# Kernel tuning notes

Measured on AMD Instinct MI355X. Metric: run time of the kernel, lower is better.

Reference implementation:

```python
import jax, jax.numpy as jnp
import numpy as np

K = 24            # neighbors
RBF_KERNELS = 16
RBF_GAMMA = 10.0
CUTOFF = 5.0
BN_EPS = 1e-5


def setup_inputs() -> dict:
    key = jax.random.key(0)
    ks = jax.random.split(key, 6)
    B, C, N = 16, 32, 2048
    x = jax.random.normal(ks[0], (B, C, N), dtype=jnp.float32)
    idx_base = (jnp.arange(B, dtype=jnp.int64) * N).reshape(B, 1, 1)
    att_w1 = jax.random.normal(ks[1], (64, 2 * C + RBF_KERNELS), dtype=jnp.float32) * 0.1
    att_w2 = jax.random.normal(ks[2], (1, 64), dtype=jnp.float32) * 0.1
    upd_w = jax.random.normal(ks[3], (64, C), dtype=jnp.float32) * 0.1
    bn_gamma = jnp.ones((64,), dtype=jnp.float32)
    bn_beta = jnp.zeros((64,), dtype=jnp.float32)
    res_w = jax.random.normal(ks[4], (64, C), dtype=jnp.float32) * 0.1
    return {"x": x, "idx_base": idx_base, "att_w1": att_w1, "att_w2": att_w2,
            "upd_w": upd_w, "bn_gamma": bn_gamma, "bn_beta": bn_beta, "res_w": res_w}


def _forward(x, att_w1, att_w2, upd_w, bn_gamma, bn_beta, res_w):
    B, C, N = x.shape
    centers = jnp.linspace(0.0, CUTOFF, RBF_KERNELS).astype(x.dtype)
    # pair[b,i,j] = -||x_i - x_j||^2  (negative squared distance)
    xx = jnp.sum(x * x, axis=1)                          # [B,N]
    dots = jnp.einsum('bcn,bcm->bnm', x, x)              # [B,N,N]
    pair = 2.0 * dots - xx[:, :, None] - xx[:, None, :]
    neg_d2, idx = jax.lax.top_k(pair, K)                 # [B,N,K] nearest neighbors
    dist = jnp.sqrt(jnp.maximum(-neg_d2, 1e-12))         # [B,N,K]
    xt = jnp.transpose(x, (0, 2, 1))                     # [B,N,C]
    neigh = xt[jnp.arange(B)[:, None, None], idx]        # [B,N,K,C] gather
    cent = jnp.broadcast_to(xt[:, :, None, :], (B, N, K, C))
    # RBF expansion of neighbor distances
    diff = dist[..., None] - centers                     # [B,N,K,RBF]
    rbf = jnp.clip(jnp.exp(-RBF_GAMMA * diff * diff), 1e-10, 1.0)
    # attention MLP (1x1 convs == per-edge dense layers)
    att_in = jnp.concatenate([cent, neigh, rbf], axis=-1)          # [B,N,K,2C+RBF]
    h = jax.nn.leaky_relu(jnp.einsum('bnkf,of->bnko', att_in, att_w1), 0.2)
    logits = jnp.einsum('bnko,o->bnk', h, att_w2[0])               # [B,N,K]
    att = jax.nn.softmax(logits, axis=-1)                          # softmax over K neighbors
    weighted = att[..., None] * neigh                              # [B,N,K,C]
    # update_ff: conv1x1 -> BatchNorm2d (batch stats over B,N,K) -> LeakyReLU(0.02)
    upd = jnp.einsum('bnkc,oc->bnko', weighted, upd_w)             # [B,N,K,64]
    mean = jnp.mean(upd, axis=(0, 1, 2))
    var = jnp.mean((upd - mean) ** 2, axis=(0, 1, 2))
    upd = (upd - mean) * jax.lax.rsqrt(var + BN_EPS) * bn_gamma + bn_beta
    upd = jax.nn.leaky_relu(upd, 0.02)
    res = jnp.einsum('bnkc,oc->bnko', neigh, res_w)                # residual projection
    feat = jnp.mean(upd + 0.1 * res, axis=2)                       # mean over K -> [B,N,64]
    return jnp.transpose(feat, (0, 2, 1))                          # [B,64,N]


def reference(x, idx_base, att_w1, att_w2, upd_w, bn_gamma, bn_beta, res_w):
    # idx_base is only needed for torch's flattened-gather trick; the per-batch
    # advanced-index gather above computes identical math.
    return _forward(x, att_w1, att_w2, upd_w, bn_gamma, bn_beta, res_w)
```

## Files before the change

### kernel.cpp

```cpp
#include <hip/hip_runtime.h>
#include <math.h>

#define B_   16
#define C_   32
#define N_   2048
#define K_   24
#define BNK_ (B_*N_*K_)

typedef float vf2 __attribute__((ext_vector_type(2)));
typedef __attribute__((ext_vector_type(8))) short bf16x8;
typedef __attribute__((ext_vector_type(4))) float f32x4;

#define WS_XT   0u
#define WS_XXD  1048576u
#define WS_XXF  1114112u
#define WS_IDX  1146880u
#define WS_D2   1933312u
#define WS_ATT  2719744u
#define WS_LOG  3506176u
#define WS_ST   4292608u
#define WS_AB   4292736u
#define WS_W    4292864u
#define WS_W2   4325632u
#define WS_Y    4358400u
#define WS_L    4358400u
#define WS_HL   10649856u

__device__ __forceinline__ unsigned short bf16rne(float f) {
  unsigned int u = __float_as_uint(f);
  return (unsigned short)((u + 0x7FFFu + ((u >> 16) & 1u)) >> 16);
}

__global__ __launch_bounds__(256) void k0_prep(const float* __restrict__ x,
                                               float* __restrict__ ws) {
  const int i = blockIdx.x;
  const int xcd = i & 7, j = i >> 3;
  const int b = 2 * xcd + (j & 1);
  const int half = j >> 1;
  const int t = (b << 11) + (half << 8) + threadIdx.x;
  const int n = t & 2047;
  const float* xp = x + ((size_t)b * C_ * N_) + n;
  float4* xt4 = (float4*)(ws + WS_XT + (size_t)t * C_);
  uint4*  hl  = (uint4*)(ws + WS_HL) + (size_t)t * 8;
  unsigned int hu[16], lu[16];
  double s = 0.0;
#pragma unroll
  for (int cg = 0; cg < 8; ++cg) {
    float4 v;
    v.x = xp[(size_t)(4*cg  ) * N_];
    v.y = xp[(size_t)(4*cg+1) * N_];
    v.z = xp[(size_t)(4*cg+2) * N_];
    v.w = xp[(size_t)(4*cg+3) * N_];
    xt4[cg] = v;
    s = fma((double)v.x, (double)v.x, s);
    s = fma((double)v.y, (double)v.y, s);
    s = fma((double)v.z, (double)v.z, s);
    s = fma((double)v.w, (double)v.w, s);
    unsigned short h0 = bf16rne(v.x), h1 = bf16rne(v.y);
    unsigned short h2 = bf16rne(v.z), h3 = bf16rne(v.w);
    float l0 = v.x - __uint_as_float((unsigned int)h0 << 16);
    float l1 = v.y - __uint_as_float((unsigned int)h1 << 16);
    float l2 = v.z - __uint_as_float((unsigned int)h2 << 16);
    float l3 = v.w - __uint_as_float((unsigned int)h3 << 16);
    hu[2*cg]   = (unsigned int)h0 | ((unsigned int)h1 << 16);
    hu[2*cg+1] = (unsigned int)h2 | ((unsigned int)h3 << 16);
    lu[2*cg]   = (unsigned int)bf16rne(l0) | ((unsigned int)bf16rne(l1) << 16);
    lu[2*cg+1] = (unsigned int)bf16rne(l2) | ((unsigned int)bf16rne(l3) << 16);
  }
#pragma unroll
  for (int q = 0; q < 4; ++q) {
    uint4 hv; hv.x = hu[4*q]; hv.y = hu[4*q+1]; hv.z = hu[4*q+2]; hv.w = hu[4*q+3];
    hl[q] = hv;
    uint4 lv; lv.x = lu[4*q]; lv.y = lu[4*q+1]; lv.z = lu[4*q+2]; lv.w = lu[4*q+3];
    hl[4+q] = lv;
  }
  ((double*)(ws + WS_XXD))[t] = s;
  ws[WS_XXF + t] = -0.5f * (float)s;
  ws[WS_W + t] = 0.f;
  ws[WS_W2 + t] = 0.f;
  if (t < 128) ws[WS_ST + t] = 0.f;
}

__global__ __launch_bounds__(256, 8) void k1a_mfma(float* __restrict__ ws) {
  __shared__ unsigned short tl[2][1024];
  const int lane = threadIdx.x & 63;
  const int wv   = __builtin_amdgcn_readfirstlane(threadIdx.x >> 6);
  const int i = blockIdx.x;
  const int xcd = i & 7, j = i >> 3;
  const int b = 2 * xcd + (j & 1);
  const int j2 = j >> 1;
  const int nblk = j2 >> 2;
  const int mq   = j2 & 3;
  const int l16 = lane & 15, lg = lane >> 4;

  const unsigned short* HL = (const unsigned short*)(ws + WS_HL) + ((size_t)b << 17);
  const int nrow = (nblk << 6) + (wv << 4) + l16;
  const bf16x8 bh = *(const bf16x8*)(HL + ((size_t)nrow << 6) + (lg << 3));
  const bf16x8 bl = *(const bf16x8*)(HL + ((size_t)nrow << 6) + 32 + (lg << 3));

  const int mbase = mq << 9;
  const float4* nxx = (const float4*)(ws + WS_XXF + (b << 11) + mbase);

  const int srow = lane >> 3;
  const int sslot = (lane & 7) ^ srow;
  const unsigned short* Sp = HL + ((size_t)(mbase + srow) << 6) + (sslot << 3);

  const int ah_off = (l16 << 6) + (((lg    ) ^ (l16 & 7)) << 3);
  const int al_off = (l16 << 6) + (((4 | lg) ^ (l16 & 7)) << 3);

  if (wv == 0) {
    __builtin_amdgcn_global_load_lds(
        (const __attribute__((address_space(1))) unsigned int*)(const void*)Sp,
        (__attribute__((address_space(3))) unsigned int*)(void*)&tl[0][0], 16, 0, 0);
    __builtin_amdgcn_global_load_lds(
        (const __attribute__((address_space(1))) unsigned int*)(const void*)(Sp + 512),
        (__attribute__((address_space(3))) unsigned int*)(void*)&tl[0][512], 16, 0, 0);
  }
  __syncthreads();

  float val[12];
#pragma unroll
  for (int j0 = 0; j0 < 12; ++j0) val[j0] = -3.4e38f;
  int id = mbase + (lg << 2);

#pragma unroll 2
  for (int t = 0; t < 32; ++t) {
    const int cur = t & 1;
    if (t < 31 && wv == (t & 3)) {
      const unsigned short* sp = Sp + ((size_t)(t + 1) << 10);
      __builtin_amdgcn_global_load_lds(
          (const __attribute__((address_space(1))) unsigned int*)(const void*)sp,
          (__attribute__((address_space(3))) unsigned int*)(void*)&tl[cur ^ 1][0], 16, 0, 0);
      __builtin_amdgcn_global_load_lds(
          (const __attribute__((address_space(1))) unsigned int*)(const void*)(sp + 512),
          (__attribute__((address_space(3))) unsigned int*)(void*)&tl[cur ^ 1][512], 16, 0, 0);
    }
    bf16x8 ah = *(const bf16x8*)(&tl[cur][ah_off]);
    bf16x8 al = *(const bf16x8*)(&tl[cur][al_off]);
    float4 xq = nxx[(t << 2) + lg];
    f32x4 acc;
    acc[0] = xq.x; acc[1] = xq.y; acc[2] = xq.z; acc[3] = xq.w;
    acc = __builtin_amdgcn_mfma_f32_16x16x32_bf16(ah, bh, acc, 0, 0, 0);
    acc = __builtin_amdgcn_mfma_f32_16x16x32_bf16(al, bh, acc, 0, 0, 0);
    acc = __builtin_amdgcn_mfma_f32_16x16x32_bf16(ah, bl, acc, 0, 0, 0);
#pragma unroll
    for (int r = 0; r < 4; ++r) {
      int sb = (__float_as_int(acc[r]) & ~2047) | (id + r);
      float sp2 = __int_as_float(sb);
#pragma unroll
      for (int j0 = 11; j0 >= 1; --j0)
        val[j0] = __builtin_amdgcn_fmed3f(val[j0 - 1], val[j0], sp2);
      val[0] = fmaxf(val[0], sp2);
    }
    id += 16;
    __syncthreads();
  }
  const int pg = (b << 5) + nblk;
  float* Lp = ws + WS_L +
      (((size_t)pg * 16 + (mq << 2) + lg) * 12) * 64 + (wv << 4) + l16;
#pragma unroll
  for (int j0 = 0; j0 < 12; ++j0) Lp[(size_t)j0 * 64] = val[j0];
}

__global__ __launch_bounds__(64) void k1b_sel(float* __restrict__ ws) {
  const float* xt = ws + WS_XT;
  const double* xxd = (const double*)(ws + WS_XXD);
  const int lane = threadIdx.x & 63;
  const int i = blockIdx.x;
  const int xcd = i & 7, j = i >> 3;
  const int b = 2 * xcd + (j & 1);
  const int sub = j >> 1;
  const int pg = (b << 5) + sub;
  const int bn = (b << 11) + (sub << 6) + lane;

  float val[28];
#pragma unroll
  for (int j0 = 0; j0 < 28; ++j0) val[j0] = -3.4e38f;
  const float* Lp = ws + WS_L + ((size_t)pg * 16 * 12) * 64 + lane;
#pragma unroll 4
  for (int t = 0; t < 192; ++t) {
    float sp = Lp[(size_t)t * 64];
#pragma unroll
    for (int j0 = 27; j0 >= 1; --j0)
      val[j0] = __builtin_amdgcn_fmed3f(val[j0 - 1], val[j0], sp);
    val[0] = fmaxf(val[0], sp);
  }

  double xnd[C_];
  {
    const float* p = xt + (size_t)bn * C_;
#pragma unroll
    for (int c = 0; c < C_; ++c) xnd[c] = (double)p[c];
  }
  double dl[K_];
#pragma unroll
  for (int j0 = 0; j0 < K_; ++j0) dl[j0] = -1.7e308;

#pragma unroll 1
  for (int j0 = 0; j0 < 28; ++j0) {
    const int m = __float_as_int(val[j0]) & 2047;
    const float* r = xt + ((size_t)((b << 11) + m)) * C_;
    double a0 = 0.0, a1 = 0.0;
#pragma unroll
    for (int c = 0; c < 16; ++c) {
      a0 = fma((double)r[c],      xnd[c],      a0);
      a1 = fma((double)r[c + 16], xnd[c + 16], a1);
    }
    double s = 2.0 * (a0 + a1) - xxd[(b << 11) + m];
    long long bits = (__double_as_longlong(s) & 0xFFFFFFFFFFFFF800ll) | (long long)m;
    double sp = __longlong_as_double(bits);
    if (sp > dl[K_ - 1]) {
      bool c2 = true;
#pragma unroll
      for (int jj = K_ - 1; jj >= 1; --jj) {
        bool c1 = sp > dl[jj - 1];
        dl[jj] = c1 ? dl[jj - 1] : (c2 ? sp : dl[jj]);
        c2 = c1;
      }
      if (c2) dl[0] = sp;
    }
  }

  int*   op = (int*)ws + WS_IDX + (size_t)bn * K_;
  float* dp = ws + WS_D2 + (size_t)bn * K_;
  const double xxn = xxd[bn];
#pragma unroll
  for (int rr = 0; rr < K_; ++rr) {
    long long bl = __double_as_longlong(dl[rr]);
    op[rr] = (int)(bl & 0x7FFll);
    dp[rr] = (float)(xxn - __longlong_as_double(bl & 0xFFFFFFFFFFFFF800ll));
  }
}

__global__ __launch_bounds__(256) void kY(const float* __restrict__ w1,
                                          const float* __restrict__ updw,
                                          const float* __restrict__ resw,
                                          float* __restrict__ ws) {
  const int lane = threadIdx.x & 63;
  const int wv   = __builtin_amdgcn_readfirstlane(threadIdx.x >> 6);
  const int i = blockIdx.x;
  const int xcd = i & 7, j = i >> 3;
  const int b = 2 * xcd + (j & 1);
  const int j2 = j >> 1;
  const int slot = (j2 << 2) | wv;
  const int s  = slot & 7;
  const int pg = slot >> 3;
  const int p = (b << 11) + (pg << 6) + lane;
  const float* xt = ws + WS_XT;

  float row[C_];
  {
    const float4* rp = (const float4*)(xt + (size_t)p * C_);
#pragma unroll
    for (int q = 0; q < 8; ++q) {
      float4 v = rp[q];
      row[4*q] = v.x; row[4*q+1] = v.y; row[4*q+2] = v.z; row[4*q+3] = v.w;
    }
  }
  const int part = s >> 1;
  const int hch  = (s & 1) * 32;
  const float* W   = (part == 0) ? w1 : (part == 1) ? (w1 + 32)
                   : (part == 2) ? updw : resw;
  const int stride = (part < 2) ? 80 : 32;
  float* yp = ws + WS_Y + (size_t)p * 256 + s * 32;
#pragma unroll 2
  for (int og = 0; og < 8; ++og) {
    float a[4] = {0.f, 0.f, 0.f, 0.f};
#pragma unroll
    for (int u = 0; u < 4; ++u) {
      const float* wr = W + (hch + 4 * og + u) * stride;
#pragma unroll
      for (int c = 0; c < C_; ++c) a[u] = fmaf(row[c], wr[c], a[u]);
    }
    float4 st; st.x = a[0]; st.y = a[1]; st.z = a[2]; st.w = a[3];
    ((float4*)yp)[og] = st;
  }
}

__global__ __launch_bounds__(256, 6) void k2_logits(const float* __restrict__ w1,
                                                    const float* __restrict__ w2,
                                                    float* __restrict__ ws) {
  const int lane = threadIdx.x & 63;
  const int wv   = __builtin_amdgcn_readfirstlane(threadIdx.x >> 6);
  const int i = blockIdx.x;
  const int xcd = i & 7, j = i >> 3;
  const int b = 2 * xcd + (j & 1);
  const int j2 = j >> 1;
  const int sub = j2 & 31;
  const int third = j2 >> 5;
  const int k0 = (third * 4 + wv) * 2;
  const int bn = (b << 11) + (sub << 6) + lane;
  const float* Y = ws + WS_Y;

  float rbf[2][16];
  int mk[2];
#pragma unroll
  for (int kk = 0; kk < 2; ++kk) {
    const int k = k0 + kk;
    mk[kk] = ((const int*)ws)[WS_IDX + (size_t)bn * K_ + k];
    const float dd = ws[WS_D2 + (size_t)bn * K_ + k];
    float dist = sqrtf(fmaxf(dd, 1e-12f));
#pragma unroll
    for (int r = 0; r < 16; ++r) {
      float t = dist - (float)r * (5.0f / 15.0f);
      float e = __expf(-10.f * t * t);
      rbf[kk][r] = fminf(fmaxf(e, 1e-10f), 1.0f);
    }
  }

  float lg[2] = {0.f, 0.f};
  const float4* bp = (const float4*)(Y + (size_t)bn * 256);
  const float4* yp0 = (const float4*)(Y + (size_t)((b << 11) + mk[0]) * 256 + 64);
  const float4* yp1 = (const float4*)(Y + (size_t)((b << 11) + mk[1]) * 256 + 64);
#pragma unroll
  for (int og = 0; og < 4; ++og) {
#pragma unroll
    for (int q = 0; q < 4; ++q) {
      float4 bv  = bp[og * 4 + q];
      float4 rv0 = yp0[og * 4 + q];
      float4 rv1 = yp1[og * 4 + q];
#pragma unroll
      for (int e = 0; e < 4; ++e) {
        const int o = og * 16 + q * 4 + e;
        const float be = (e == 0) ? bv.x : (e == 1) ? bv.y : (e == 2) ? bv.z : bv.w;
        const float r0 = (e == 0) ? rv0.x : (e == 1) ? rv0.y : (e == 2) ? rv0.z : rv0.w;
        const float r1 = (e == 0) ? rv1.x : (e == 1) ? rv1.y : (e == 2) ? rv1.z : rv1.w;
        float a0 = be + r0, a1 = be + r1;
#pragma unroll
        for (int r = 0; r < 16; ++r) {
          const float wv1 = w1[o * 80 + 64 + r];
          a0 = fmaf(rbf[0][r], wv1, a0);
          a1 = fmaf(rbf[1][r], wv1, a1);
        }
        float h0 = a0 > 0.f ? a0 : 0.2f * a0;
        float h1 = a1 > 0.f ? a1 : 0.2f * a1;
        lg[0] = fmaf(h0, w2[o], lg[0]);
        lg[1] = fmaf(h1, w2[o], lg[1]);
      }
    }
  }
#pragma unroll
  for (int kk = 0; kk < 2; ++kk)
    ws[WS_LOG + (size_t)(k0 + kk) * 32768 + bn] = lg[kk];
}

__global__ __launch_bounds__(256) void k2_softmax(float* __restrict__ ws) {
  __shared__ float h[4096];
  const int i = blockIdx.x;
  const int xcd = i & 7, j = i >> 3;
  const int b = 2 * xcd + (j & 1);
  const int half = j >> 1;
  const int bn = (b << 11) + (half << 8) + threadIdx.x;

#pragma unroll
  for (int q = 0; q < 16; ++q) h[threadIdx.x + (q << 8)] = 0.f;
  __syncthreads();

  float l[K_];
#pragma unroll
  for (int k = 0; k < K_; ++k) l[k] = ws[WS_LOG + (size_t)k * 32768 + bn];
  float mx = l[0];
#pragma unroll
  for (int k = 1; k < K_; ++k) mx = fmaxf(mx, l[k]);
  float den = 0.f;
#pragma unroll
  for (int k = 0; k < K_; ++k) { l[k] = __expf(l[k] - mx); den += l[k]; }
  const float inv = 1.f / den;
#pragma unroll
  for (int k = 0; k < K_; ++k) l[k] *= inv;

  float4* ap = (float4*)(ws + WS_ATT + (size_t)bn * K_);
#pragma unroll
  for (int q = 0; q < 6; ++q) {
    float4 v; v.x = l[4*q]; v.y = l[4*q+1]; v.z = l[4*q+2]; v.w = l[4*q+3];
    ap[q] = v;
  }
  const int* ip = (const int*)ws + WS_IDX + (size_t)bn * K_;
#pragma unroll
  for (int k = 0; k < K_; ++k) {
    const int mk = ip[k];
    atomicAdd(&h[mk], l[k]);
    atomicAdd(&h[2048 + mk], l[k] * l[k]);
  }
  __syncthreads();
#pragma unroll
  for (int q = 0; q < 8; ++q) {
    const int m = threadIdx.x + (q << 8);
    atomicAdd(ws + WS_W  + (b << 11) + m, h[m]);
    atomicAdd(ws + WS_W2 + (b << 11) + m, h[2048 + m]);
  }
}

__global__ __launch_bounds__(256) void k2b_stats(float* __restrict__ ws) {
  __shared__ float ls[128];
  const int lane = threadIdx.x & 63;
  const int wv   = __builtin_amdgcn_readfirstlane(threadIdx.x >> 6);
  if (threadIdx.x < 128) ls[threadIdx.x] = 0.f;
  __syncthreads();
  const int i = blockIdx.x;
  const int xcd = i & 7, j = i >> 3;
  const int b = 2 * xcd + (j & 1);
  const int half = j >> 1;
  const float* Y = ws + WS_Y;
  float s1 = 0.f, s2 = 0.f;
#pragma unroll 1
  for (int it = 0; it < 64; ++it) {
    const int m = (b << 11) + (half << 8) + (wv << 6) + it;
    const float w  = ws[WS_W + m];
    const float w2 = ws[WS_W2 + m];
    const float yv = Y[(size_t)m * 256 + 128 + lane];
    s1 = fmaf(w, yv, s1);
    s2 = fmaf(w2, yv * yv, s2);
  }
  atomicAdd(&ls[lane], s1);
  atomicAdd(&ls[64 + lane], s2);
  __syncthreads();
  if (threadIdx.x < 128) atomicAdd(ws + WS_ST + threadIdx.x, ls[threadIdx.x]);
}

__global__ __launch_bounds__(256) void k4_out(float* __restrict__ out,
                                              const float* __restrict__ gam,
                                              const float* __restrict__ bet,
                                              const float* __restrict__ ws) {
  __shared__ float tile[32][65];
  const int lane = threadIdx.x & 63;
  const int wv   = __builtin_amdgcn_readfirstlane(threadIdx.x >> 6);
  const int i = blockIdx.x;
  const int xcd = i & 7, j = i >> 3;
  const int b = 2 * xcd + (j & 1);
  const int j2 = j >> 1;
  const int n0 = j2 << 5;
  const float* Y = ws + WS_Y;

  float A, Bb;
  {
    const float s1 = ws[WS_ST + lane], s2 = ws[WS_ST + 64 + lane];
    const float cnt = (float)BNK_;
    const float mean = s1 / cnt;
    const float var = fmaxf(s2 / cnt - mean * mean, 0.f);
    A = gam[lane] / sqrtf(var + 1e-5f);
    Bb = bet[lane] - mean * A;
  }

#pragma unroll 1
  for (int pt = 0; pt < 8; ++pt) {
    const int bn = (b << 11) + n0 + (wv << 3) + pt;
    const int*   ip = (const int*)ws + WS_IDX + (size_t)bn * K_;
    const float* ap = ws + WS_ATT + (size_t)bn * K_;
    float facc = 0.f, racc = 0.f;
#pragma unroll
    for (int k = 0; k < K_; ++k) {
      const int mk = ip[k];
      const float* row = Y + (size_t)((b << 11) + mk) * 256;
      float yv = row[128 + lane];
      float rv = row[192 + lane];
      float u = ap[k] * yv;
      float v = fmaf(u, A, Bb);
      v = v > 0.f ? v : 0.02f * v;
      facc += v;
      racc += rv;
    }
    tile[(wv << 3) + pt][lane] = (facc + 0.1f * racc) * (1.f / 24.f);
  }
  __syncthreads();
  const int o = threadIdx.x >> 2, q = threadIdx.x & 3;
  float* op = out + ((size_t)(b * 64 + o)) * 2048 + n0 + q * 8;
  float4 v0, v1;
  v0.x = tile[q*8+0][o]; v0.y = tile[q*8+1][o]; v0.z = tile[q*8+2][o]; v0.w = tile[q*8+3][o];
  v1.x = tile[q*8+4][o]; v1.y = tile[q*8+5][o]; v1.z = tile[q*8+6][o]; v1.w = tile[q*8+7][o];
  ((float4*)op)[0] = v0;
  ((float4*)op)[1] = v1;
}

extern "C" void kernel_launch(void* const* d_in, const int* in_sizes, int n_in,
                              void* d_out, int out_size, void* d_ws, size_t ws_size,
                              hipStream_t stream) {
  (void)in_sizes; (void)n_in; (void)out_size; (void)ws_size;
  const float* x    = (const float*)d_in[0];
  const float* w1   = (const float*)d_in[2];
  const float* w2   = (const float*)d_in[3];
  const float* updw = (const float*)d_in[4];
  const float* bng  = (const float*)d_in[5];
  const float* bnb  = (const float*)d_in[6];
  const float* resw = (const float*)d_in[7];
  float* out = (float*)d_out;
  float* ws  = (float*)d_ws;

  k0_prep  <<<dim3(128),  dim3(256), 0, stream>>>(x, ws);
  k1a_mfma <<<dim3(2048), dim3(256), 0, stream>>>(ws);
  k1b_sel  <<<dim3(512),  dim3(64),  0, stream>>>(ws);
  kY       <<<dim3(1024), dim3(256), 0, stream>>>(w1, updw, resw, ws);
  k2_logits<<<dim3(1536), dim3(256), 0, stream>>>(w1, w2, ws);
  k2_softmax<<<dim3(128), dim3(256), 0, stream>>>(ws);
  k2b_stats<<<dim3(128),  dim3(256), 0, stream>>>(ws);
  k4_out   <<<dim3(1024), dim3(256), 0, stream>>>(out, bng, bnb, ws);
}
```

Baseline: 328.0 us.

## Split logits hidden dim across 16 lanes with weights in registers and shuffle reduce

Restructures the attention-logit kernel so each point is handled by 16 lanes, each owning 4 of the 64 hidden channels. Each lane keeps its slice of the RBF weights and w2 in registers and loops over all 24 neighbors. The 64-wide hidden reduction is done with xor shuffles. This replaces the per-lane loop over every hidden output, which reloaded w1 scalars and read full 256-byte Y rows per neighbor, with coalesced float4 slices. The cost is that every lane recomputes the 16 RBF exponentials redundantly, plus shuffle overhead, a changed grid size and a lower occupancy hint.

```diff
diff --git a/kernel.cpp b/kernel.cpp
--- a/kernel.cpp
+++ b/kernel.cpp
@@ -277,71 +277,67 @@
   }
 }
 
-__global__ __launch_bounds__(256, 6) void k2_logits(const float* __restrict__ w1,
+__global__ __launch_bounds__(256, 4) void k2_logits(const float* __restrict__ w1,
                                                     const float* __restrict__ w2,
                                                     float* __restrict__ ws) {
   const int lane = threadIdx.x & 63;
   const int wv   = __builtin_amdgcn_readfirstlane(threadIdx.x >> 6);
-  const int i = blockIdx.x;
-  const int xcd = i & 7, j = i >> 3;
-  const int b = 2 * xcd + (j & 1);
-  const int j2 = j >> 1;
-  const int sub = j2 & 31;
-  const int third = j2 >> 5;
-  const int k0 = (third * 4 + wv) * 2;
-  const int bn = (b << 11) + (sub << 6) + lane;
+  const int s = lane & 15, g = lane >> 4;
+  const int i = blockIdx.x;
+  const int xcd = i & 7, j = i >> 3;
+  const int b = 2 * xcd + (j & 1);
+  const int grp = j >> 1;
+  const int bn = (b << 11) + (grp << 4) + (wv << 2) + g;
   const float* Y = ws + WS_Y;
 
-  float rbf[2][16];
-  int mk[2];
-#pragma unroll
-  for (int kk = 0; kk < 2; ++kk) {
-    const int k = k0 + kk;
-    mk[kk] = ((const int*)ws)[WS_IDX + (size_t)bn * K_ + k];
-    const float dd = ws[WS_D2 + (size_t)bn * K_ + k];
-    float dist = sqrtf(fmaxf(dd, 1e-12f));
+  float w1r[4][16], w2r[4], ba[4];
+#pragma unroll
+  for (int e = 0; e < 4; ++e) {
+    const int o = 4 * s + e;
+    w2r[e] = w2[o];
+#pragma unroll
+    for (int q = 0; q < 4; ++q) {
+      float4 v = *(const float4*)(w1 + o * 80 + 64 + 4 * q);
+      w1r[e][4*q] = v.x; w1r[e][4*q+1] = v.y; w1r[e][4*q+2] = v.z; w1r[e][4*q+3] = v.w;
+    }
+  }
+  {
+    float4 v = *(const float4*)(Y + (size_t)bn * 256 + 4 * s);
+    ba[0] = v.x; ba[1] = v.y; ba[2] = v.z; ba[3] = v.w;
+  }
+
+  const int*   ip = (const int*)ws + WS_IDX + (size_t)bn * K_;
+  const float* dp = ws + WS_D2 + (size_t)bn * K_;
+
+#pragma unroll 2
+  for (int k = 0; k < K_; ++k) {
+    const int mk  = ip[k];
+    const float dd = dp[k];
+    const float dist = sqrtf(fmaxf(dd, 1e-12f));
+    float4 rv = *(const float4*)(Y + (size_t)((b << 11) + mk) * 256 + 64 + 4 * s);
+    float a0 = ba[0] + rv.x, a1 = ba[1] + rv.y, a2 = ba[2] + rv.z, a3 = ba[3] + rv.w;
 #pragma unroll
     for (int r = 0; r < 16; ++r) {
       float t = dist - (float)r * (5.0f / 15.0f);
       float e = __expf(-10.f * t * t);
-      rbf[kk][r] = fminf(fmaxf(e, 1e-10f), 1.0f);
-    }
-  }
-
-  float lg[2] = {0.f, 0.f};
-  const float4* bp = (const float4*)(Y + (size_t)bn * 256);
-  const float4* yp0 = (const float4*)(Y + (size_t)((b << 11) + mk[0]) * 256 + 64);
-  const float4* yp1 = (const float4*)(Y + (size_t)((b << 11) + mk[1]) * 256 + 64);
-#pragma unroll
-  for (int og = 0; og < 4; ++og) {
-#pragma unroll
-    for (int q = 0; q < 4; ++q) {
-      float4 bv  = bp[og * 4 + q];
-      float4 rv0 = yp0[og * 4 + q];
-      float4 rv1 = yp1[og * 4 + q];
-#pragma unroll
-      for (int e = 0; e < 4; ++e) {
-        const int o = og * 16 + q * 4 + e;
-        const float be = (e == 0) ? bv.x : (e == 1) ? bv.y : (e == 2) ? bv.z : bv.w;
-        const float r0 = (e == 0) ? rv0.x : (e == 1) ? rv0.y : (e == 2) ? rv0.z : rv0.w;
-        const float r1 = (e == 0) ? rv1.x : (e == 1) ? rv1.y : (e == 2) ? rv1.z : rv1.w;
-        float a0 = be + r0, a1 = be + r1;
-#pragma unroll
-        for (int r = 0; r < 16; ++r) {
-          const float wv1 = w1[o * 80 + 64 + r];
-          a0 = fmaf(rbf[0][r], wv1, a0);
-          a1 = fmaf(rbf[1][r], wv1, a1);
-        }
-        float h0 = a0 > 0.f ? a0 : 0.2f * a0;
-        float h1 = a1 > 0.f ? a1 : 0.2f * a1;
-        lg[0] = fmaf(h0, w2[o], lg[0]);
-        lg[1] = fmaf(h1, w2[o], lg[1]);
-      }
-    }
-  }
-#pragma unroll
-  for (int kk = 0; kk < 2; ++kk)
-    ws[WS_LOG + (size_t)(k0 + kk) * 32768 + bn] = lg[kk];
+      float rb = fminf(fmaxf(e, 1e-10f), 1.0f);
+      a0 = fmaf(rb, w1r[0][r], a0);
+      a1 = fmaf(rb, w1r[1][r], a1);
+      a2 = fmaf(rb, w1r[2][r], a2);
+      a3 = fmaf(rb, w1r[3][r], a3);
+    }
+    a0 = fmaxf(a0, 0.2f * a0); a1 = fmaxf(a1, 0.2f * a1);
+    a2 = fmaxf(a2, 0.2f * a2); a3 = fmaxf(a3, 0.2f * a3);
+    float p = a0 * w2r[0];
+    p = fmaf(a1, w2r[1], p);
+    p = fmaf(a2, w2r[2], p);
+    p = fmaf(a3, w2r[3], p);
+    p += __shfl_xor(p, 1);
+    p += __shfl_xor(p, 2);
+    p += __shfl_xor(p, 4);
+    p += __shfl_xor(p, 8);
+    if (s == 0) ws[WS_LOG + (size_t)k * 32768 + bn] = p;
+  }
 }
 
 __global__ __launch_bounds__(256) void k2_softmax(float* __restrict__ ws) {
@@ -490,7 +486,7 @@
   k1a_mfma <<<dim3(2048), dim3(256), 0, stream>>>(ws);
   k1b_sel  <<<dim3(512),  dim3(64),  0, stream>>>(ws);
   kY       <<<dim3(1024), dim3(256), 0, stream>>>(w1, updw, resw, ws);
-  k2_logits<<<dim3(1536), dim3(256), 0, stream>>>(w1, w2, ws);
+  k2_logits<<<dim3(2048), dim3(256), 0, stream>>>(w1, w2, ws);
   k2_softmax<<<dim3(128), dim3(256), 0, stream>>>(ws);
   k2b_stats<<<dim3(128),  dim3(256), 0, stream>>>(ws);
   k4_out   <<<dim3(1024), dim3(256), 0, stream>>>(out, bng, bnb, ws);
```

Result: slower. 348.2 us (+6.2%).
